# Performance work log

Hardware: AMD Instinct MI355X
Metric: run time of the kernel (lower is better)

Reference implementation:

```python
import jax, jax.numpy as jnp
import numpy as np


def setup_inputs() -> dict:
    key = jax.random.key(0)
    ks = jax.random.split(key, 9)
    B, C, H, W = 4, 256, 128, 128
    d = C // 8
    x = jax.random.normal(ks[0], (B, C, H, W), jnp.float32)
    wq = jax.random.normal(ks[1], (d, C), jnp.float32) * 0.05
    bq = jax.random.normal(ks[2], (d,), jnp.float32) * 0.05
    wk = jax.random.normal(ks[3], (d, C), jnp.float32) * 0.05
    bk = jax.random.normal(ks[4], (d,), jnp.float32) * 0.05
    wv = jax.random.normal(ks[5], (d, C), jnp.float32) * 0.05
    bv = jax.random.normal(ks[6], (d,), jnp.float32) * 0.05
    wp = jax.random.normal(ks[7], (C, d, 3, 3), jnp.float32) * 0.05
    gamma = jax.random.normal(ks[8], (1,), jnp.float32)
    return dict(x=x, wq=wq, bq=bq, wk=wk, bk=bk, wv=wv, bv=bv, wp=wp, gamma=gamma)


def reference(x, wq, bq, wk, bk, wv, bv, wp, gamma):
    B, C, H, W = x.shape
    d = wq.shape[0]  # C // 8
    N = H * W
    # 1x1 convs expressed as channel matmuls
    q = jnp.einsum('bchw,dc->bdhw', x, wq) + bq[None, :, None, None]
    k = jnp.einsum('bchw,dc->bdhw', x, wk) + bk[None, :, None, None]
    v = jnp.einsum('bchw,dc->bdhw', x, wv) + bv[None, :, None, None]
    Q = q.reshape(B, d, N)
    K = k.reshape(B, d, N)
    V = v.reshape(B, d, N)
    # channel-channel energy: [B, d, d]
    energy = jnp.einsum('bdn,ben->bde', Q, K)
    energy_new = jnp.max(energy, axis=-1, keepdims=True) - energy
    attention = jax.nn.softmax(energy_new, axis=-1)
    out = jnp.einsum('bde,ben->bdn', attention, V).reshape(B, d, H, W)
    # 3x3 conv (no bias) + exact GELU
    out = jax.lax.conv_general_dilated(
        out, wp, window_strides=(1, 1), padding='SAME',
        dimension_numbers=('NCHW', 'OIHW', 'NCHW'))
    out = jax.nn.gelu(out, approximate=False)
    return gamma[0] * out + x
```

## Files before the change

### kernel.cpp

```cpp
#include <hip/hip_runtime.h>
#include <hip/hip_bf16.h>
#include <math.h>

#define BB 4
#define CC 256
#define HH 128
#define WW 128
#define NN (HH*WW)
#define DD 32

#define AOT_CI   44
#define AOT_ROWE (130*AOT_CI)
#define AOT_IMGE (130*AOT_ROWE)
#define AOT_BYTES ((size_t)BB*AOT_IMGE*2)
#define AOT_ALLOC (AOT_BYTES + 1024)

#define WT_BYTES (9*256*AOT_CI*2)

#define PATCH_SZ 45760
#define WSLAB    22528
#define CONV_LDS (PATCH_SZ + 2*WSLAB)
#define EPI_PITCH 260

#define BPITCH 272
#define AQ_OFF 69632
#define ACH    26112
#define APACK_BYTES (4*2*ACH)
#define QKP    260

typedef __attribute__((ext_vector_type(8))) short bf16x8;
typedef __attribute__((ext_vector_type(4))) float f32x4;

__device__ inline void async_copy16(void* lds, const void* g) {
    __builtin_amdgcn_global_load_lds(
        (const __attribute__((address_space(1))) unsigned int*)g,
        (__attribute__((address_space(3))) unsigned int*)lds, 16, 0, 0);
}

__device__ inline unsigned short f2bf(float f) {
    __hip_bfloat16 h = __float2bfloat16(f);
    return *reinterpret_cast<unsigned short*>(&h);
}

__device__ inline void split2(float v, unsigned short& h, unsigned short& l) {
    __hip_bfloat16 hb = __float2bfloat16(v);
    float r = v - __bfloat162float(hb);
    __hip_bfloat16 lb = __float2bfloat16(r);
    h = *reinterpret_cast<unsigned short*>(&hb);
    l = *reinterpret_cast<unsigned short*>(&lb);
}

__device__ inline bf16x8 ld_frag8(const char* p) {
    union { bf16x8 v; short4 h[2]; } u;
    u.h[0] = *(const short4*)(p);
    u.h[1] = *(const short4*)(p + 8);
    return u.v;
}

__device__ inline float gelu_fast(float v) {
    float a = fabsf(v) * 0.70710678118654752f;
    float t = __fdividef(1.0f, fmaf(0.3275911f, a, 1.0f));
    float p = t * fmaf(t, fmaf(t, fmaf(t, fmaf(t, 1.061405429f, -1.453152027f),
                                       1.421413741f), -0.284496736f), 0.254829592f);
    float e = 1.0f - p * __expf(-a * a);
    float erfv = (v < 0.0f) ? -e : e;
    return 0.5f * v * (1.0f + erfv);
}

__global__ __launch_bounds__(256) void wrepack2_kernel(
    const float* __restrict__ wq, const float* __restrict__ wk,
    const float* __restrict__ wv, unsigned short* __restrict__ Apack)
{
    int i = blockIdx.x * 256 + threadIdx.x;
    if (i >= 4*96*68) return;
    int q = i / (96*68);
    int r = i % (96*68);
    int m = r / 68, j = r % 68;
    unsigned short h = 0, l = 0;
    if (j < 64) {
        int c = 64*q + j;
        float w = (m < 32) ? wq[m*256 + c]
                : (m < 64) ? wk[(m-32)*256 + c]
                           : wv[(m-64)*256 + c];
        split2(w, h, l);
    }
    size_t oh = ((size_t)(q*2 + 0)*96 + m)*136 + 2*j;
    size_t ol = ((size_t)(q*2 + 1)*96 + m)*136 + 2*j;
    Apack[oh] = h; Apack[oh+1] = h;
    Apack[ol] = l; Apack[ol+1] = l;
}

__global__ __launch_bounds__(512, 1) void qkv_mfma_kernel(
    const float* __restrict__ x, const unsigned short* __restrict__ Apack,
    const float* __restrict__ bq, const float* __restrict__ bk,
    const float* __restrict__ bv,
    float* __restrict__ Vout, float* __restrict__ Ep)
{
    __shared__ __align__(16) char lds[AQ_OFF + 2*ACH];
    __shared__ float biasL[96];
    const int b   = blockIdx.y;
    const int s   = blockIdx.x;
    const int n0  = s * 256;
    const int tid = threadIdx.x;
    const int lane = tid & 63;
    const int wid  = tid >> 6;
    const int wm = wid >> 2, wn = wid & 3;
    const int l15 = lane & 15, lj = lane >> 4;

    if (tid < 96)
        biasL[tid] = (tid < 32) ? bq[tid] : (tid < 64) ? bk[tid-32] : bv[tid-64];

    const float* xb = x + (size_t)b*CC*NN + n0;

    f32x4 acc[3][4];
    #pragma unroll
    for (int cf = 0; cf < 3; ++cf)
        #pragma unroll
        for (int nf = 0; nf < 4; ++nf)
            acc[cf][nf] = (f32x4){0.f, 0.f, 0.f, 0.f};

    for (int q = 0; q < 4; ++q) {
        __syncthreads();
        {
            const char* src = (const char*)Apack + (size_t)q*2*ACH;
            for (int i = tid; i < 3264; i += 512)
                async_copy16(lds + AQ_OFF + i*16, src + i*16);
        }
        for (int i = tid; i < 4096; i += 512) {
            int cq = i >> 8, n = i & 255;
            const float* xp = xb + (size_t)(64*q + 4*cq)*NN + n;
            float x0 = xp[0], x1 = xp[NN], x2 = xp[2*NN], x3 = xp[3*NN];
            union { bf16x8 v; unsigned short u[8]; } pk;
            split2(x0, pk.u[0], pk.u[1]);
            split2(x1, pk.u[2], pk.u[3]);
            split2(x2, pk.u[4], pk.u[5]);
            split2(x3, pk.u[6], pk.u[7]);
            *(bf16x8*)(lds + n*BPITCH + cq*16) = pk.v;
        }
        __syncthreads();
        const char* Ah = lds + AQ_OFF;
        const char* Al = lds + AQ_OFF + ACH;
        #pragma unroll
        for (int st = 0; st < 4; ++st) {
            const int ko = lj*16 + st*64;
            bf16x8 bf[4];
            #pragma unroll
            for (int nf = 0; nf < 4; ++nf)
                bf[nf] = *(const bf16x8*)(lds + (64*wn + 16*nf + l15)*BPITCH + ko);
            #pragma unroll
            for (int cf = 0; cf < 3; ++cf) {
                const int arow = (48*wm + 16*cf + l15)*BPITCH + ko;
                bf16x8 ah = *(const bf16x8*)(Ah + arow);
                bf16x8 al = *(const bf16x8*)(Al + arow);
                #pragma unroll
                for (int nf = 0; nf < 4; ++nf) {
                    acc[cf][nf] = __builtin_amdgcn_mfma_f32_16x16x32_bf16(
                        ah, bf[nf], acc[cf][nf], 0, 0, 0);
                    acc[cf][nf] = __builtin_amdgcn_mfma_f32_16x16x32_bf16(
                        al, bf[nf], acc[cf][nf], 0, 0, 0);
                }
            }
        }
    }

    __syncthreads();
    float* qk = (float*)lds;
    #pragma unroll
    for (int cf = 0; cf < 3; ++cf) {
        const int rbase = 48*wm + 16*cf + 4*lj;
        #pragma unroll
        for (int nf = 0; nf < 4; ++nf) {
            const int col = 64*wn + 16*nf + l15;
            #pragma unroll
            for (int j = 0; j < 4; ++j) {
                const int row = rbase + j;
                const float v = acc[cf][nf][j] + biasL[row];
                if (row < 64)
                    qk[row*QKP + col] = v;
                else
                    Vout[((size_t)b*DD + (row-64))*NN + n0 + col] = v;
            }
        }
    }
    __syncthreads();

    const int d  = tid >> 4;
    const int e0 = tid & 15;
    const float* qrow = qk + d*QKP;
    const float* ka   = qk + (32 + e0)*QKP;
    const float* kb   = qk + (48 + e0)*QKP;
    float s0 = 0.f, s1 = 0.f;
    for (int n4 = 0; n4 < 256; n4 += 4) {
        float4 qv = *(const float4*)(qrow + n4);
        float4 va = *(const float4*)(ka + n4);
        float4 vb = *(const float4*)(kb + n4);
        s0 += qv.x*va.x + qv.y*va.y + qv.z*va.z + qv.w*va.w;
        s1 += qv.x*vb.x + qv.y*vb.y + qv.z*vb.z + qv.w*vb.w;
    }
    float* ep = Ep + ((size_t)s*BB + b)*1024;
    ep[d*32 + e0]      = s0;
    ep[d*32 + e0 + 16] = s1;
}

__global__ __launch_bounds__(1024) void softmax_kernel(
    const float* __restrict__ Ep, float* __restrict__ attT)
{
    const int b = blockIdx.x;
    const int e = threadIdx.x, d = threadIdx.y;
    float s = 0.f;
    for (int p = 0; p < 64; ++p)
        s += Ep[((size_t)p * BB + b) * (DD * DD) + d * DD + e];
    float nv = -s;
    float m = nv;
    for (int off = 16; off > 0; off >>= 1) m = fmaxf(m, __shfl_xor(m, off, 32));
    float pe = expf(nv - m);
    float su = pe;
    for (int off = 16; off > 0; off >>= 1) su += __shfl_xor(su, off, 32);
    attT[(size_t)b * (DD * DD) + e * DD + d] = pe / su;
}

__global__ __launch_bounds__(256) void pv_kernel(
    const float* __restrict__ V, const float* __restrict__ attT,
    unsigned short* __restrict__ AOT)
{
    __shared__ float Vs[DD][256];
    __shared__ float at4[DD][DD];
    const int b  = blockIdx.y;
    const int n0 = blockIdx.x * 256;
    for (int i = threadIdx.x; i < DD * 256; i += 256) {
        int r = i >> 8, cc = i & 255;
        Vs[r][cc] = V[((size_t)b*DD + r)*NN + n0 + cc];
    }
    for (int i = threadIdx.x; i < DD * DD; i += 256)
        at4[i >> 5][i & 31] = attT[(size_t)b * (DD * DD) + i];
    __syncthreads();
    const int t = threadIdx.x;
    float acc[DD];
    #pragma unroll
    for (int d = 0; d < DD; ++d) acc[d] = 0.f;
    #pragma unroll 4
    for (int e = 0; e < DD; ++e) {
        float v = Vs[e][t];
        const float4* ar = (const float4*)at4[e];
        #pragma unroll
        for (int dq = 0; dq < 8; ++dq) {
            float4 a = ar[dq];
            acc[4*dq+0] += a.x * v; acc[4*dq+1] += a.y * v;
            acc[4*dq+2] += a.z * v; acc[4*dq+3] += a.w * v;
        }
    }
    const int n = n0 + t;
    const int h = n >> 7, w = n & 127;
    unsigned short* dst = AOT + (size_t)b*AOT_IMGE + (size_t)(h+1)*AOT_ROWE
                              + (size_t)(w+1)*AOT_CI;
    #pragma unroll
    for (int dq = 0; dq < 8; ++dq) {
        ushort4 u;
        u.x = f2bf(acc[4*dq+0]); u.y = f2bf(acc[4*dq+1]);
        u.z = f2bf(acc[4*dq+2]); u.w = f2bf(acc[4*dq+3]);
        *(ushort4*)(dst + 4*dq) = u;
    }
}

__global__ __launch_bounds__(256) void wrepack_kernel(
    const float* __restrict__ wp, unsigned short* __restrict__ Wt)
{
    int i = blockIdx.x * 256 + threadIdx.x;
    if (i >= 9*256*32) return;
    int kk = i / (256*32);
    int r  = i % (256*32);
    int co = r >> 5, ci = r & 31;
    float v = wp[((size_t)co*32 + ci)*9 + kk];
    Wt[((size_t)kk*256 + co)*AOT_CI + ci] = f2bf(v);
}

__global__ __launch_bounds__(512, 1) void conv_kernel(
    const unsigned short* __restrict__ AOT, const unsigned short* __restrict__ Wt,
    const float* __restrict__ gammap, const float* __restrict__ x,
    float* __restrict__ out)
{
    __shared__ __align__(16) char lds[CONV_LDS];
    const int b   = blockIdx.y;
    const int h0  = blockIdx.x * 2;
    const int tid = threadIdx.x;
    const int wid = tid >> 6;
    const int lane = tid & 63;
    const int l15 = lane & 15;
    const int lj  = lane >> 4;
    const int wn  = wid & 1;
    const int wc  = wid >> 1;

    const char* psrc = (const char*)(AOT + (size_t)b*AOT_IMGE + (size_t)h0*AOT_ROWE);
    for (int i = tid; i < PATCH_SZ/16; i += 512)
        async_copy16(lds + i*16, psrc + i*16);
    for (int i = tid; i < WSLAB/16; i += 512)
        async_copy16(lds + PATCH_SZ + i*16, (const char*)Wt + i*16);
    __syncthreads();

    f32x4 acc[4][8];
    #pragma unroll
    for (int cf = 0; cf < 4; ++cf)
        #pragma unroll
        for (int nf = 0; nf < 8; ++nf)
            acc[cf][nf] = (f32x4){0.f, 0.f, 0.f, 0.f};

    for (int kk = 0; kk < 9; ++kk) {
        if (kk < 8) {
            const char* wsrc = (const char*)Wt + (size_t)(kk+1)*WSLAB;
            char* wdst = lds + PATCH_SZ + ((kk+1)&1)*WSLAB;
            for (int i = tid; i < WSLAB/16; i += 512)
                async_copy16(wdst + i*16, wsrc + i*16);
        }
        const int kh = kk / 3, kw = kk % 3;
        const char* wbase = lds + PATCH_SZ + (kk&1)*WSLAB;
        bf16x8 af[4];
        #pragma unroll
        for (int cf = 0; cf < 4; ++cf)
            af[cf] = ld_frag8(wbase + (wc*64 + cf*16 + l15)*88 + lj*16);
        #pragma unroll
        for (int nf = 0; nf < 8; ++nf) {
            const int cell = (wn + kh)*130 + nf*16 + l15 + kw;
            const bf16x8 bfr = ld_frag8(lds + cell*88 + lj*16);
            #pragma unroll
            for (int cf = 0; cf < 4; ++cf)
                acc[cf][nf] = __builtin_amdgcn_mfma_f32_16x16x32_bf16(
                    af[cf], bfr, acc[cf][nf], 0, 0, 0);
        }
        __syncthreads();
    }

    const float g0 = gammap[0];
    float* lf = (float*)lds;
    for (int k = 0; k < 4; ++k) {
        if (wc == k) {
            #pragma unroll
            for (int cf = 0; cf < 4; ++cf) {
                const int rl = cf*16 + 4*lj;
                #pragma unroll
                for (int nf = 0; nf < 8; ++nf) {
                    const int col = wn*128 + nf*16 + l15;
                    #pragma unroll
                    for (int j = 0; j < 4; ++j)
                        lf[(rl + j)*EPI_PITCH + col] = acc[cf][nf][j];
                }
            }
        }
        __syncthreads();
        #pragma unroll
        for (int it = 0; it < 8; ++it) {
            const int idx = tid + it*512;
            const int row = idx >> 6, c4 = idx & 63;
            const int co  = k*64 + row;
            const size_t g = ((size_t)b*CC + co)*NN + (size_t)h0*WW + c4*4;
            float4 v  = *(const float4*)(lf + row*EPI_PITCH + c4*4);
            float4 xv = *(const float4*)(x + g);
            float4 o;
            o.x = g0*gelu_fast(v.x) + xv.x;
            o.y = g0*gelu_fast(v.y) + xv.y;
            o.z = g0*gelu_fast(v.z) + xv.z;
            o.w = g0*gelu_fast(v.w) + xv.w;
            *(float4*)(out + g) = o;
        }
        __syncthreads();
    }
}

extern "C" void kernel_launch(void* const* d_in, const int* in_sizes, int n_in,
                              void* d_out, int out_size, void* d_ws, size_t ws_size,
                              hipStream_t stream)
{
    const float* x  = (const float*)d_in[0];
    const float* wq = (const float*)d_in[1];
    const float* bq = (const float*)d_in[2];
    const float* wk = (const float*)d_in[3];
    const float* bk = (const float*)d_in[4];
    const float* wv = (const float*)d_in[5];
    const float* bv = (const float*)d_in[6];
    const float* wp = (const float*)d_in[7];
    const float* gm = (const float*)d_in[8];
    float* out = (float*)d_out;

    float* Vbuf = out;

    char* ws = (char*)d_ws;
    unsigned short* AOT   = (unsigned short*)ws;
    unsigned short* Wt    = (unsigned short*)(ws + AOT_ALLOC);
    unsigned short* Apack = (unsigned short*)(ws + AOT_ALLOC + WT_BYTES);
    float* Ep  = (float*)(ws + AOT_ALLOC + WT_BYTES + APACK_BYTES);
    float* ATT = Ep + 64*BB*1024;

    hipMemsetAsync(AOT, 0, AOT_ALLOC, stream);
    wrepack_kernel <<<dim3(288), 256, 0, stream>>>(wp, Wt);
    wrepack2_kernel<<<dim3((4*96*68 + 255)/256), 256, 0, stream>>>(wq, wk, wv, Apack);
    qkv_mfma_kernel<<<dim3(64, BB), 512, 0, stream>>>(x, Apack, bq, bk, bv, Vbuf, Ep);
    softmax_kernel <<<dim3(BB), dim3(32, 32), 0, stream>>>(Ep, ATT);
    pv_kernel      <<<dim3(NN/256, BB), 256, 0, stream>>>(Vbuf, ATT, AOT);
    conv_kernel    <<<dim3(64, BB), 512, 0, stream>>>(AOT, Wt, gm, x, out);
}
```

Measured before the change: 93.30 us.

## Restructure QKV projection to 32x32 MFMA with register-fed x and pre-swizzled weights

The QKV projection kernel now loads the whole pre-swizzled split-bf16 weight matrix into LDS once. Each wave computes 32 columns with 32x32x16 MFMAs, building the B operand straight from registers and prefetching x values four steps ahead. This removes the per-quarter LDS staging of x and its barriers. The hipMemsetAsync is also replaced by a custom zero kernel. The cost is a larger register footprint and a weight layout tied to this exact shape.

```diff
diff --git a/kernel.cpp b/kernel.cpp
--- a/kernel.cpp
+++ b/kernel.cpp
@@ -22,14 +22,12 @@
 #define CONV_LDS (PATCH_SZ + 2*WSLAB)
 #define EPI_PITCH 260
 
-#define BPITCH 272
-#define AQ_OFF 69632
-#define ACH    26112
-#define APACK_BYTES (4*2*ACH)
-#define QKP    260
-
-typedef __attribute__((ext_vector_type(8))) short bf16x8;
-typedef __attribute__((ext_vector_type(4))) float f32x4;
+#define ASWZ_BYTES 98304
+#define QKP 260
+
+typedef __attribute__((ext_vector_type(8)))  short bf16x8;
+typedef __attribute__((ext_vector_type(4)))  float f32x4;
+typedef __attribute__((ext_vector_type(16))) float f32x16;
 
 __device__ inline void async_copy16(void* lds, const void* g) {
     __builtin_amdgcn_global_load_lds(
@@ -67,119 +65,117 @@
     return 0.5f * v * (1.0f + erfv);
 }
 
+__global__ __launch_bounds__(256) void zero_kernel(uint4* __restrict__ p, int n16)
+{
+    for (int i = blockIdx.x*256 + threadIdx.x; i < n16; i += gridDim.x*256)
+        p[i] = (uint4){0u, 0u, 0u, 0u};
+}
+
 __global__ __launch_bounds__(256) void wrepack2_kernel(
     const float* __restrict__ wq, const float* __restrict__ wk,
-    const float* __restrict__ wv, unsigned short* __restrict__ Apack)
-{
-    int i = blockIdx.x * 256 + threadIdx.x;
-    if (i >= 4*96*68) return;
-    int q = i / (96*68);
-    int r = i % (96*68);
-    int m = r / 68, j = r % 68;
-    unsigned short h = 0, l = 0;
-    if (j < 64) {
-        int c = 64*q + j;
-        float w = (m < 32) ? wq[m*256 + c]
-                : (m < 64) ? wk[(m-32)*256 + c]
-                           : wv[(m-64)*256 + c];
-        split2(w, h, l);
-    }
-    size_t oh = ((size_t)(q*2 + 0)*96 + m)*136 + 2*j;
-    size_t ol = ((size_t)(q*2 + 1)*96 + m)*136 + 2*j;
-    Apack[oh] = h; Apack[oh+1] = h;
-    Apack[ol] = l; Apack[ol+1] = l;
+    const float* __restrict__ wv, unsigned short* __restrict__ Aswz)
+{
+    int i = blockIdx.x*256 + threadIdx.x;
+    if (i >= 49152) return;
+    int j    = i & 7;
+    int lane = (i >> 3) & 63;
+    int cf   = (i >> 9) % 3;
+    int s    = i / 1536;
+    int row  = cf*32 + (lane & 31);
+    int k    = s*16 + (lane >> 5)*8 + j;
+    int c    = k >> 1;
+    float w  = (row < 32) ? wq[row*256 + c]
+             : (row < 64) ? wk[(row-32)*256 + c]
+                          : wv[(row-64)*256 + c];
+    unsigned short h, l;
+    split2(w, h, l);
+    Aswz[i] = (k & 1) ? l : h;
 }
 
 __global__ __launch_bounds__(512, 1) void qkv_mfma_kernel(
-    const float* __restrict__ x, const unsigned short* __restrict__ Apack,
+    const float* __restrict__ x, const unsigned short* __restrict__ Aswz,
     const float* __restrict__ bq, const float* __restrict__ bk,
     const float* __restrict__ bv,
     float* __restrict__ Vout, float* __restrict__ Ep)
 {
-    __shared__ __align__(16) char lds[AQ_OFF + 2*ACH];
+    __shared__ __align__(16) char lds[ASWZ_BYTES];
     __shared__ float biasL[96];
-    const int b   = blockIdx.y;
-    const int s   = blockIdx.x;
-    const int n0  = s * 256;
-    const int tid = threadIdx.x;
+    const int b    = blockIdx.y;
+    const int s    = blockIdx.x;
+    const int n0   = s * 256;
+    const int tid  = threadIdx.x;
     const int lane = tid & 63;
     const int wid  = tid >> 6;
-    const int wm = wid >> 2, wn = wid & 3;
-    const int l15 = lane & 15, lj = lane >> 4;
-
+    const int l31  = lane & 31;
+    const int lh   = lane >> 5;
+    const int nloc = 32*wid + l31;
+
+    for (int i = tid; i < 6144; i += 512)
+        async_copy16(lds + i*16, (const char*)Aswz + i*16);
     if (tid < 96)
         biasL[tid] = (tid < 32) ? bq[tid] : (tid < 64) ? bk[tid-32] : bv[tid-64];
 
-    const float* xb = x + (size_t)b*CC*NN + n0;
-
-    f32x4 acc[3][4];
-    #pragma unroll
-    for (int cf = 0; cf < 3; ++cf)
-        #pragma unroll
-        for (int nf = 0; nf < 4; ++nf)
-            acc[cf][nf] = (f32x4){0.f, 0.f, 0.f, 0.f};
-
-    for (int q = 0; q < 4; ++q) {
-        __syncthreads();
+    const float* xlane = x + ((size_t)b*CC + 4*lh)*NN + (n0 + nloc);
+
+    f32x16 acc0 = {0}, acc1 = {0}, acc2 = {0};
+
+    float xq[4][4];
+    #pragma unroll
+    for (int p0 = 0; p0 < 4; ++p0) {
+        const float* p = xlane + (size_t)(8*p0)*NN;
+        xq[p0][0] = p[0];            xq[p0][1] = p[(size_t)NN];
+        xq[p0][2] = p[(size_t)2*NN]; xq[p0][3] = p[(size_t)3*NN];
+    }
+
+    __syncthreads();
+
+    for (int su = 0; su < 32; su += 4) {
+        #pragma unroll
+        for (int ph = 0; ph < 4; ++ph) {
+            const int st = su + ph;
+            const char* ab = lds + (size_t)(st*3)*1024 + lane*16;
+            bf16x8 a0 = *(const bf16x8*)(ab);
+            bf16x8 a1 = *(const bf16x8*)(ab + 1024);
+            bf16x8 a2 = *(const bf16x8*)(ab + 2048);
+            float xv0 = xq[ph][0], xv1 = xq[ph][1];
+            float xv2 = xq[ph][2], xv3 = xq[ph][3];
+            if (st + 4 < 32) {
+                const float* p = xlane + (size_t)(8*(st+4))*NN;
+                xq[ph][0] = p[0];            xq[ph][1] = p[(size_t)NN];
+                xq[ph][2] = p[(size_t)2*NN]; xq[ph][3] = p[(size_t)3*NN];
+            }
+            union { bf16x8 v; unsigned short u[8]; } B1, B2;
+            unsigned short h, l;
+            split2(xv0, h, l); B1.u[0] = h; B1.u[1] = h; B2.u[0] = l; B2.u[1] = l;
+            split2(xv1, h, l); B1.u[2] = h; B1.u[3] = h; B2.u[2] = l; B2.u[3] = l;
+            split2(xv2, h, l); B1.u[4] = h; B1.u[5] = h; B2.u[4] = l; B2.u[5] = l;
+            split2(xv3, h, l); B1.u[6] = h; B1.u[7] = h; B2.u[6] = l; B2.u[7] = l;
+
+            acc0 = __builtin_amdgcn_mfma_f32_32x32x16_bf16(a0, B1.v, acc0, 0, 0, 0);
+            acc1 = __builtin_amdgcn_mfma_f32_32x32x16_bf16(a1, B1.v, acc1, 0, 0, 0);
+            acc2 = __builtin_amdgcn_mfma_f32_32x32x16_bf16(a2, B1.v, acc2, 0, 0, 0);
+            acc0 = __builtin_amdgcn_mfma_f32_32x32x16_bf16(a0, B2.v, acc0, 0, 0, 0);
+            acc1 = __builtin_amdgcn_mfma_f32_32x32x16_bf16(a1, B2.v, acc1, 0, 0, 0);
+            acc2 = __builtin_amdgcn_mfma_f32_32x32x16_bf16(a2, B2.v, acc2, 0, 0, 0);
+        }
+    }
+
+    __syncthreads();
+    float* qk = (float*)lds;
+    #pragma unroll
+    for (int r = 0; r < 16; ++r) {
+        const int rsub = (r & 3) + 8*(r >> 2) + 4*lh;
         {
-            const char* src = (const char*)Apack + (size_t)q*2*ACH;
-            for (int i = tid; i < 3264; i += 512)
-                async_copy16(lds + AQ_OFF + i*16, src + i*16);
-        }
-        for (int i = tid; i < 4096; i += 512) {
-            int cq = i >> 8, n = i & 255;
-            const float* xp = xb + (size_t)(64*q + 4*cq)*NN + n;
-            float x0 = xp[0], x1 = xp[NN], x2 = xp[2*NN], x3 = xp[3*NN];
-            union { bf16x8 v; unsigned short u[8]; } pk;
-            split2(x0, pk.u[0], pk.u[1]);
-            split2(x1, pk.u[2], pk.u[3]);
-            split2(x2, pk.u[4], pk.u[5]);
-            split2(x3, pk.u[6], pk.u[7]);
-            *(bf16x8*)(lds + n*BPITCH + cq*16) = pk.v;
-        }
-        __syncthreads();
-        const char* Ah = lds + AQ_OFF;
-        const char* Al = lds + AQ_OFF + ACH;
-        #pragma unroll
-        for (int st = 0; st < 4; ++st) {
-            const int ko = lj*16 + st*64;
-            bf16x8 bf[4];
-            #pragma unroll
-            for (int nf = 0; nf < 4; ++nf)
-                bf[nf] = *(const bf16x8*)(lds + (64*wn + 16*nf + l15)*BPITCH + ko);
-            #pragma unroll
-            for (int cf = 0; cf < 3; ++cf) {
-                const int arow = (48*wm + 16*cf + l15)*BPITCH + ko;
-                bf16x8 ah = *(const bf16x8*)(Ah + arow);
-                bf16x8 al = *(const bf16x8*)(Al + arow);
-                #pragma unroll
-                for (int nf = 0; nf < 4; ++nf) {
-                    acc[cf][nf] = __builtin_amdgcn_mfma_f32_16x16x32_bf16(
-                        ah, bf[nf], acc[cf][nf], 0, 0, 0);
-                    acc[cf][nf] = __builtin_amdgcn_mfma_f32_16x16x32_bf16(
-                        al, bf[nf], acc[cf][nf], 0, 0, 0);
-                }
-            }
-        }
-    }
-
-    __syncthreads();
-    float* qk = (float*)lds;
-    #pragma unroll
-    for (int cf = 0; cf < 3; ++cf) {
-        const int rbase = 48*wm + 16*cf + 4*lj;
-        #pragma unroll
-        for (int nf = 0; nf < 4; ++nf) {
-            const int col = 64*wn + 16*nf + l15;
-            #pragma unroll
-            for (int j = 0; j < 4; ++j) {
-                const int row = rbase + j;
-                const float v = acc[cf][nf][j] + biasL[row];
-                if (row < 64)
-                    qk[row*QKP + col] = v;
-                else
-                    Vout[((size_t)b*DD + (row-64))*NN + n0 + col] = v;
-            }
+            const int row = rsub;
+            qk[row*QKP + nloc] = acc0[r] + biasL[row];
+        }
+        {
+            const int row = 32 + rsub;
+            qk[row*QKP + nloc] = acc1[r] + biasL[row];
+        }
+        {
+            const int row = 64 + rsub;
+            Vout[((size_t)b*DD + rsub)*NN + n0 + nloc] = acc2[r] + biasL[row];
         }
     }
     __syncthreads();
@@ -383,16 +379,16 @@
     float* Vbuf = out;
 
     char* ws = (char*)d_ws;
-    unsigned short* AOT   = (unsigned short*)ws;
-    unsigned short* Wt    = (unsigned short*)(ws + AOT_ALLOC);
-    unsigned short* Apack = (unsigned short*)(ws + AOT_ALLOC + WT_BYTES);
-    float* Ep  = (float*)(ws + AOT_ALLOC + WT_BYTES + APACK_BYTES);
+    unsigned short* AOT  = (unsigned short*)ws;
+    unsigned short* Wt   = (unsigned short*)(ws + AOT_ALLOC);
+    unsigned short* Aswz = (unsigned short*)(ws + AOT_ALLOC + WT_BYTES);
+    float* Ep  = (float*)(ws + AOT_ALLOC + WT_BYTES + ASWZ_BYTES);
     float* ATT = Ep + 64*BB*1024;
 
-    hipMemsetAsync(AOT, 0, AOT_ALLOC, stream);
+    zero_kernel    <<<dim3(1024), 256, 0, stream>>>((uint4*)AOT, (int)(AOT_ALLOC/16));
     wrepack_kernel <<<dim3(288), 256, 0, stream>>>(wp, Wt);
-    wrepack2_kernel<<<dim3((4*96*68 + 255)/256), 256, 0, stream>>>(wq, wk, wv, Apack);
-    qkv_mfma_kernel<<<dim3(64, BB), 512, 0, stream>>>(x, Apack, bq, bk, bv, Vbuf, Ep);
+    wrepack2_kernel<<<dim3(192), 256, 0, stream>>>(wq, wk, wv, Aswz);
+    qkv_mfma_kernel<<<dim3(64, BB), 512, 0, stream>>>(x, Aswz, bq, bk, bv, Vbuf, Ep);
     softmax_kernel <<<dim3(BB), dim3(32, 32), 0, stream>>>(Ep, ATT);
     pv_kernel      <<<dim3(NN/256, BB), 256, 0, stream>>>(Vbuf, ATT, AOT);
     conv_kernel    <<<dim3(64, BB), 512, 0, stream>>>(AOT, Wt, gm, x, out);
```

Measured after the change: 84.39 us. 1.11x faster.
